# Performance work log

Hardware: AMD Instinct MI355X
Metric: run time of the kernel (lower is better)

## Reference

```python
import jax, jax.numpy as jnp
import numpy as np

ODIM = 8192      # output dim (slice target)
MSIZE = 64       # tile size
N_BLOCKS = 1024  # size of shared block bank


def setup_inputs() -> dict:
    key = jax.random.key(0)
    k1, k2, k3, k4 = jax.random.split(key, 4)
    x = jax.random.normal(k1, (256, 8192), dtype=jnp.float32)
    # bank of msize x msize module blocks (scaled like fan-in init)
    blocks = jax.random.normal(k2, (N_BLOCKS, MSIZE, MSIZE), dtype=jnp.float32) * 0.02
    bound = 1.0 / np.sqrt(ODIM).astype(np.float32)
    bias = jax.random.uniform(k3, (ODIM,), dtype=jnp.float32, minval=-bound, maxval=bound)
    # parts: [icount, ocount] indices into the block bank
    parts = jax.random.randint(k4, (128, 128), 0, N_BLOCKS)
    return {"x": x, "blocks": blocks, "bias": bias, "parts": parts}


def reference(x, blocks, bias, parts):
    icount, ocount = parts.shape
    m = blocks.shape[-1]
    # build_mosaic: gather blocks per parts and tile into a dense weight matrix
    fc = blocks[parts]                                   # [ic, oc, m, m]
    fc_mat = fc.transpose(0, 2, 1, 3).reshape(icount * m, ocount * m)
    # idim (8192) is divisible by msize, so pad is identity (rem == 0 branch)
    y = x @ fc_mat                                       # [B, oc*m]
    y = y[..., :ODIM] + bias                             # slice + bias; post = Identity
    return y
```

## Files before the change

### kernel.cpp

```cpp
#include <hip/hip_runtime.h>
#include <stdint.h>

#define BATCH 256
#define IDIM  8192
#define ODIM  8192
#define MS    64
#define IC    128
#define OC    128
#define NB    1024

#define BM 256
#define BN 256
#define BK 64
#define KSPLIT 8
#define KT (IC / KSPLIT)

#define ABUF(s) ((s) * 16384)
#define BBUF(s) (32768 + (s) * 16384)

typedef __bf16 bf16x8 __attribute__((ext_vector_type(8)));
typedef float  floatx4 __attribute__((ext_vector_type(4)));

#define WAITCNT_VM(n) ((((n) & 15) | (((n) >> 4) << 14)) | 0x70 | 0xF00)

__device__ __forceinline__ void async_load16(unsigned short* lds_p, const unsigned short* g_p) {
    __builtin_amdgcn_global_load_lds(
        (const __attribute__((address_space(1))) unsigned int*)g_p,
        (__attribute__((address_space(3))) unsigned int*)lds_p,
        16, 0, 0);
}

__device__ __forceinline__ unsigned short f32_to_bf16(float f) {
    unsigned int u = __float_as_uint(f);
    u += 0x7FFFu + ((u >> 16) & 1u);
    return (unsigned short)(u >> 16);
}

#define XCONV_BLKS 1024
#define PT_BLKS 64
__global__ void k_convert(const float* __restrict__ x, const float* __restrict__ blocks,
                          const int* __restrict__ parts,
                          unsigned short* __restrict__ xb, unsigned short* __restrict__ bt,
                          int* __restrict__ pT) {
    __shared__ float tile[MS][MS + 1];
    int b = blockIdx.x;
    if (b < NB) {
        const float4* src4 = (const float4*)(blocks + (size_t)b * MS * MS);
        unsigned short* dst = bt + (size_t)b * MS * MS;
        #pragma unroll
        for (int i = 0; i < 4; ++i) {
            int slot = i * 256 + threadIdx.x;
            int r = slot >> 4, c4 = (slot & 15) * 4;
            float4 v = src4[slot];
            tile[r][c4 + 0] = v.x; tile[r][c4 + 1] = v.y;
            tile[r][c4 + 2] = v.z; tile[r][c4 + 3] = v.w;
        }
        __syncthreads();
        #pragma unroll
        for (int i = 0; i < 2; ++i) {
            int slot = i * 256 + threadIdx.x;
            int c = slot >> 3, o = slot & 7;
            union { unsigned short s[8]; uint4 v; } u;
            #pragma unroll
            for (int j = 0; j < 8; ++j) u.s[j] = f32_to_bf16(tile[o * 8 + j][c]);
            *(uint4*)(dst + c * MS + o * 8) = u.v;
        }
    } else if (b < NB + XCONV_BLKS) {
        int t = (b - NB) * 256 + threadIdx.x;
        const float4* x4 = (const float4*)x;
        float4 a = x4[2 * t], bb = x4[2 * t + 1];
        union { unsigned short s[8]; uint4 v; } u;
        u.s[0] = f32_to_bf16(a.x);  u.s[1] = f32_to_bf16(a.y);
        u.s[2] = f32_to_bf16(a.z);  u.s[3] = f32_to_bf16(a.w);
        u.s[4] = f32_to_bf16(bb.x); u.s[5] = f32_to_bf16(bb.y);
        u.s[6] = f32_to_bf16(bb.z); u.s[7] = f32_to_bf16(bb.w);
        ((uint4*)xb)[t] = u.v;
    } else {
        int t = (b - NB - XCONV_BLKS) * 256 + threadIdx.x;
        int oc = t >> 7, ic = t & 127;
        pT[t] = parts[ic * OC + oc];
    }
}

extern __shared__ unsigned short smem[];

__global__ __launch_bounds__(512, 2)
void k_mosaic_gemm(const unsigned short* __restrict__ xb,
                   const unsigned short* __restrict__ bt,
                   const int* __restrict__ pT,
                   float* __restrict__ partial) {
    const int tid  = threadIdx.x;
    const int lane = tid & 63;
    const int wave = tid >> 6;
    const int wrow = wave >> 2;
    const int wcol = wave & 3;
    const int ks = blockIdx.x;
    const int nt = blockIdx.y;

    const int ob0 = nt * 4;
    const int kb0 = ks * KT;

    const int row  = lane & 15;
    const int quad = lane >> 4;

    int pv = pT[(ob0 + quad) * IC + kb0 + row];

    const int swz0 = ((quad)     ^ (row & 7)) << 3;
    const int swz1 = ((quad + 4) ^ (row & 7)) << 3;
    const int a_b0 = (wrow * 128 + row) * MS + swz0;
    const int a_b1 = (wrow * 128 + row) * MS + swz1;
    const int b_b0 = (wcol * 64 + row) * MS + swz0;
    const int b_b1 = (wcol * 64 + row) * MS + swz1;

    floatx4 acc[8][4];
    #pragma unroll
    for (int mi = 0; mi < 8; ++mi)
        #pragma unroll
        for (int ni = 0; ni < 4; ++ni)
            acc[mi][ni] = (floatx4){0.f, 0.f, 0.f, 0.f};

    bf16x8 af[4], bfr[4];

#define STAGE_A(dstS, kb) do {                                                \
    _Pragma("unroll")                                                         \
    for (int j = 0; j < 4; ++j) {                                             \
        int slot = j * 512 + tid;               \
        int m = slot >> 3;                                                    \
        int oct = (slot & 7) ^ (m & 7);                                       \
        async_load16(smem + ABUF(dstS) + slot * 8,                            \
                     xb + (size_t)m * IDIM + (kb) * MS + oct * 8);            \
    } } while (0)

#define STAGE_B(dstS, tt) do {                                                \
    _Pragma("unroll")                                                         \
    for (int j = 0; j < 4; ++j) {                                             \
        int q = __shfl(pv, j * 16 + (tt));                                    \
        int slot = j * 512 + tid;                                             \
        int n = slot >> 3;                                                    \
        int oct = (slot & 7) ^ (n & 7);                                       \
        async_load16(smem + BBUF(dstS) + slot * 8,                            \
                     bt + (size_t)q * (MS * MS) + (n & 63) * MS + oct * 8);   \
    } } while (0)

#define BARRIER_PIN() do {                                                    \
    __builtin_amdgcn_sched_barrier(0);                                        \
    __builtin_amdgcn_s_barrier();                                             \
    __builtin_amdgcn_sched_barrier(0); } while (0)

#define LOAD_A(S, abase, mh) do {                                             \
    _Pragma("unroll")                                                         \
    for (int mi = 0; mi < 4; ++mi)                                            \
        af[mi] = *(const bf16x8*)(smem + ABUF(S) + (abase) + (mh) * 4096 + mi * 1024); \
    } while (0)

#define LOAD_B(S, bbase) do {                                                 \
    _Pragma("unroll")                                                         \
    for (int ni = 0; ni < 4; ++ni)                                            \
        bfr[ni] = *(const bf16x8*)(smem + BBUF(S) + (bbase) + ni * 1024);     \
    } while (0)

#define MFMA16(mh) do {                                                       \
    __builtin_amdgcn_s_setprio(1);                                            \
    _Pragma("unroll")                                                         \
    for (int mi = 0; mi < 4; ++mi)                                            \
        _Pragma("unroll")                                                     \
        for (int ni = 0; ni < 4; ++ni)                                        \
            acc[(mh) * 4 + mi][ni] = __builtin_amdgcn_mfma_f32_16x16x32_bf16( \
                af[mi], bfr[ni], acc[(mh) * 4 + mi][ni], 0, 0, 0);            \
    __builtin_amdgcn_s_setprio(0); } while (0)

#define TILE(t, AS, BS, AN, BN2, STA, STB, WN) do {                           \
                                      \
    LOAD_A(AS, a_b0, 0); LOAD_B(BS, b_b0);                                    \
    if (STA) STAGE_A(AN, kb0 + (t) + 1);                                      \
    BARRIER_PIN();                                                            \
    MFMA16(0);                                                                \
    BARRIER_PIN();                                                            \
                                      \
    LOAD_A(AS, a_b0, 1);                                                      \
    if (STB) STAGE_B(BN2, (t) + 2);                                           \
    BARRIER_PIN();                                                            \
    MFMA16(1);                                                                \
    BARRIER_PIN();                                                            \
                                                        \
    LOAD_A(AS, a_b1, 0); LOAD_B(BS, b_b1);                                    \
    BARRIER_PIN();                                                            \
    MFMA16(0);                                                                \
    BARRIER_PIN();                                                            \
             \
    LOAD_A(AS, a_b1, 1);                                                      \
    BARRIER_PIN();                                                            \
    MFMA16(1);                                                                \
    __builtin_amdgcn_sched_barrier(0);                                        \
    if ((WN) >= 0) __builtin_amdgcn_s_waitcnt(WAITCNT_VM((WN) & 63));         \
    __builtin_amdgcn_s_barrier();                                             \
    __builtin_amdgcn_sched_barrier(0);                                        \
    } while (0)

    STAGE_A(0, kb0);
    STAGE_B(0, 0);
    STAGE_B(1, 1);
    __builtin_amdgcn_sched_barrier(0);
    __builtin_amdgcn_s_waitcnt(WAITCNT_VM(4));
    __builtin_amdgcn_s_barrier();
    __builtin_amdgcn_sched_barrier(0);

    #pragma unroll 1
    for (int t6 = 0; t6 < 12; t6 += 6) {
        TILE(t6 + 0, 0, 0, 1, 2, 1, 1, 4);
        TILE(t6 + 1, 1, 1, 0, 0, 1, 1, 4);
        TILE(t6 + 2, 0, 2, 1, 1, 1, 1, 4);
        TILE(t6 + 3, 1, 0, 0, 2, 1, 1, 4);
        TILE(t6 + 4, 0, 1, 1, 0, 1, 1, 4);
        TILE(t6 + 5, 1, 2, 0, 1, 1, 1, 4);
    }
    TILE(12, 0, 0, 1, 2, 1, 1, 4);
    TILE(13, 1, 1, 0, 0, 1, 1, 4);
    TILE(14, 0, 2, 1, 0, 1, 0, 0);
    TILE(15, 1, 0, 0, 0, 0, 0, -1);

    float* out = partial + (size_t)ks * ((size_t)BATCH * ODIM);
    #pragma unroll
    for (int mi8 = 0; mi8 < 8; ++mi8)
        #pragma unroll
        for (int ni = 0; ni < 4; ++ni)
            #pragma unroll
            for (int r = 0; r < 4; ++r) {
                int rowg = wrow * 128 + mi8 * 16 + quad * 4 + r;
                int colg = nt * BN + wcol * 64 + ni * 16 + row;
                out[(size_t)rowg * ODIM + colg] = acc[mi8][ni][r];
            }
}

__global__ void k_reduce_bias(const float* __restrict__ partial,
                              const float* __restrict__ bias,
                              float* __restrict__ out) {
    int t = blockIdx.x * 256 + threadIdx.x;
    const float4* b4 = (const float4*)bias;
    float4 c = b4[t & (ODIM / 4 - 1)];
    float4 r = {c.x, c.y, c.z, c.w};
    #pragma unroll
    for (int k = 0; k < KSPLIT; ++k) {
        const float4* p = (const float4*)(partial + (size_t)k * BATCH * ODIM);
        float4 a = p[t];
        r.x += a.x; r.y += a.y; r.z += a.z; r.w += a.w;
    }
    ((float4*)out)[t] = r;
}

extern "C" void kernel_launch(void* const* d_in, const int* in_sizes, int n_in,
                              void* d_out, int out_size, void* d_ws, size_t ws_size,
                              hipStream_t stream) {
    const float* x      = (const float*)d_in[0];
    const float* blocks = (const float*)d_in[1];
    const float* bias   = (const float*)d_in[2];
    const int*   parts  = (const int*)d_in[3];
    float* out = (float*)d_out;

    char* ws = (char*)d_ws;
    unsigned short* xb      = (unsigned short*)ws;
    unsigned short* btb     = (unsigned short*)(ws + (4u << 20));
    int*            pTr     = (int*)(ws + (12u << 20));
    float*          partial = (float*)(ws + (13u << 20));

    static bool attr_set = false;
    if (!attr_set) {
        hipFuncSetAttribute((const void*)k_mosaic_gemm,
                            hipFuncAttributeMaxDynamicSharedMemorySize, 160 * 1024);
        attr_set = true;
    }

    k_convert<<<NB + XCONV_BLKS + PT_BLKS, 256, 0, stream>>>(x, blocks, parts, xb, btb, pTr);
    k_mosaic_gemm<<<dim3(KSPLIT, ODIM / BN), 512, 160 * 1024, stream>>>(xb, btb, pTr, partial);
    k_reduce_bias<<<(BATCH * ODIM) / (256 * 4), 256, 0, stream>>>(partial, bias, out);
}
```

Baseline: 128.0 us.

## Drop intra-tile barriers and issue next-stage prefetches before compute

Each K-tile used to be split into four LDS-load/MFMA phases, each fenced by workgroup barriers, with setprio raised around the MFMA runs. Now each tile first issues the async global-to-LDS prefetches for later stages, waits with a deeper vmcnt threshold, takes one barrier, then runs all LDS reads and MFMAs freely with a single trailing barrier. This removes about eight barriers per tile and lets the compiler interleave LDS reads with MFMAs. In exchange it gives up the explicit ping-pong style scheduling and priority hints, which may have been hiding memory latency across waves.

```diff
diff --git a/kernel.cpp b/kernel.cpp
--- a/kernel.cpp
+++ b/kernel.cpp
@@ -142,11 +142,6 @@
                      bt + (size_t)q * (MS * MS) + (n & 63) * MS + oct * 8);   \
     } } while (0)
 
-#define BARRIER_PIN() do {                                                    \
-    __builtin_amdgcn_sched_barrier(0);                                        \
-    __builtin_amdgcn_s_barrier();                                             \
-    __builtin_amdgcn_sched_barrier(0); } while (0)
-
 #define LOAD_A(S, abase, mh) do {                                             \
     _Pragma("unroll")                                                         \
     for (int mi = 0; mi < 4; ++mi)                                            \
@@ -160,39 +155,30 @@
     } while (0)
 
 #define MFMA16(mh) do {                                                       \
-    __builtin_amdgcn_s_setprio(1);                                            \
     _Pragma("unroll")                                                         \
     for (int mi = 0; mi < 4; ++mi)                                            \
         _Pragma("unroll")                                                     \
         for (int ni = 0; ni < 4; ++ni)                                        \
             acc[(mh) * 4 + mi][ni] = __builtin_amdgcn_mfma_f32_16x16x32_bf16( \
                 af[mi], bfr[ni], acc[(mh) * 4 + mi][ni], 0, 0, 0);            \
-    __builtin_amdgcn_s_setprio(0); } while (0)
+    } while (0)
+
+#define COMPUTE(AS, BS) do {                                                  \
+    LOAD_A(AS, a_b0, 0); LOAD_B(BS, b_b0); MFMA16(0);                         \
+    LOAD_A(AS, a_b0, 1);                   MFMA16(1);                         \
+    LOAD_A(AS, a_b1, 0); LOAD_B(BS, b_b1); MFMA16(0);                         \
+    LOAD_A(AS, a_b1, 1);                   MFMA16(1);                         \
+    } while (0)
 
 #define TILE(t, AS, BS, AN, BN2, STA, STB, WN) do {                           \
-                                      \
-    LOAD_A(AS, a_b0, 0); LOAD_B(BS, b_b0);                                    \
     if (STA) STAGE_A(AN, kb0 + (t) + 1);                                      \
-    BARRIER_PIN();                                                            \
-    MFMA16(0);                                                                \
-    BARRIER_PIN();                                                            \
-                                      \
-    LOAD_A(AS, a_b0, 1);                                                      \
     if (STB) STAGE_B(BN2, (t) + 2);                                           \
-    BARRIER_PIN();                                                            \
-    MFMA16(1);                                                                \
-    BARRIER_PIN();                                                            \
-                                                        \
-    LOAD_A(AS, a_b1, 0); LOAD_B(BS, b_b1);                                    \
-    BARRIER_PIN();                                                            \
-    MFMA16(0);                                                                \
-    BARRIER_PIN();                                                            \
-             \
-    LOAD_A(AS, a_b1, 1);                                                      \
-    BARRIER_PIN();                                                            \
-    MFMA16(1);                                                                \
-    __builtin_amdgcn_sched_barrier(0);                                        \
-    if ((WN) >= 0) __builtin_amdgcn_s_waitcnt(WAITCNT_VM((WN) & 63));         \
+    __builtin_amdgcn_sched_barrier(0);                                        \
+    __builtin_amdgcn_s_waitcnt(WAITCNT_VM(WN));                               \
+    __builtin_amdgcn_s_barrier();                                             \
+    __builtin_amdgcn_sched_barrier(0);                                        \
+    COMPUTE(AS, BS);                                                          \
+    __builtin_amdgcn_sched_barrier(0);                                        \
     __builtin_amdgcn_s_barrier();                                             \
     __builtin_amdgcn_sched_barrier(0);                                        \
     } while (0)
@@ -200,24 +186,20 @@
     STAGE_A(0, kb0);
     STAGE_B(0, 0);
     STAGE_B(1, 1);
-    __builtin_amdgcn_sched_barrier(0);
-    __builtin_amdgcn_s_waitcnt(WAITCNT_VM(4));
-    __builtin_amdgcn_s_barrier();
-    __builtin_amdgcn_sched_barrier(0);
 
     #pragma unroll 1
     for (int t6 = 0; t6 < 12; t6 += 6) {
-        TILE(t6 + 0, 0, 0, 1, 2, 1, 1, 4);
-        TILE(t6 + 1, 1, 1, 0, 0, 1, 1, 4);
-        TILE(t6 + 2, 0, 2, 1, 1, 1, 1, 4);
-        TILE(t6 + 3, 1, 0, 0, 2, 1, 1, 4);
-        TILE(t6 + 4, 0, 1, 1, 0, 1, 1, 4);
-        TILE(t6 + 5, 1, 2, 0, 1, 1, 1, 4);
-    }
-    TILE(12, 0, 0, 1, 2, 1, 1, 4);
-    TILE(13, 1, 1, 0, 0, 1, 1, 4);
-    TILE(14, 0, 2, 1, 0, 1, 0, 0);
-    TILE(15, 1, 0, 0, 0, 0, 0, -1);
+        TILE(t6 + 0, 0, 0, 1, 2, 1, 1, 12);
+        TILE(t6 + 1, 1, 1, 0, 0, 1, 1, 12);
+        TILE(t6 + 2, 0, 2, 1, 1, 1, 1, 12);
+        TILE(t6 + 3, 1, 0, 0, 2, 1, 1, 12);
+        TILE(t6 + 4, 0, 1, 1, 0, 1, 1, 12);
+        TILE(t6 + 5, 1, 2, 0, 1, 1, 1, 12);
+    }
+    TILE(12, 0, 0, 1, 2, 1, 1, 12);
+    TILE(13, 1, 1, 0, 0, 1, 1, 12);
+    TILE(14, 0, 2, 1, 0, 1, 0, 8);
+    TILE(15, 1, 0, 0, 0, 0, 0, 0);
 
     float* out = partial + (size_t)ks * ((size_t)BATCH * ODIM);
     #pragma unroll
```

Measured after the change: 128.6 us. Within noise of the previous version (+0.5%).
